# Performance work log

Hardware: AMD Instinct MI355X
Metric: run time of the kernel (lower is better)

Reference implementation:

```python
import jax, jax.numpy as jnp
import numpy as np

# LocalConv config (must match init_kwargs)
B, C, H, W = 64, 16, 64, 64
KH, KW = 3, 3
SH, SW = 1, 1
OUT_CH = 32
OH = (H - KH + SH) // SH  # 62
OW = (W - KW + SW) // SW  # 62
P = OH * OW               # 3844 positions
FEAT = C * KH * KW        # 144 (flatten order: C, kh, kw)


def setup_inputs() -> dict:
    key = jax.random.key(0)
    k1, k2 = jax.random.split(key)
    inputs = jax.random.normal(k1, (B, C, H, W), dtype=jnp.float32)
    kernel = jax.random.normal(k2, (P, FEAT, OUT_CH), dtype=jnp.float32)
    return {"inputs": inputs, "kernel": kernel}


def _extract_patches(x):
    # x: (B, C, H, W) -> (P, B, FEAT) with FEAT flattened as (C, kh, kw),
    # matching torch's reshape of inputs[:, :, i:i+kh, j:j+kw].
    i_idx = (jnp.arange(OH) * SH)[:, None] + jnp.arange(KH)[None, :]  # (OH, KH)
    j_idx = (jnp.arange(OW) * SW)[:, None] + jnp.arange(KW)[None, :]  # (OW, KW)
    # gather -> (B, C, OH, KH, OW, KW)
    p = x[:, :, i_idx[:, :, None, None], j_idx[None, None, :, :]]
    # -> (OH, OW, B, C, KH, KW)
    p = jnp.transpose(p, (2, 4, 0, 1, 3, 5))
    return p.reshape(P, B, FEAT)


def reference(inputs, kernel):
    patches = _extract_patches(inputs)                 # (P, B, FEAT)
    out = jnp.einsum('pbf,pfo->pbo', patches, kernel)  # per-position unshared matmul
    out = out.reshape(OH, OW, B, OUT_CH)
    return jnp.transpose(out, (2, 3, 0, 1))            # (B, OUT_CH, OH, OW)
```

## Files before the change

kernel.cpp:

```cpp
#include <hip/hip_runtime.h>

#define CIN    16
#define HH     64
#define WW     64
#define OHD    62
#define OWD    62
#define OUTC   32
#define FEATN  144
#define POUT   (OHD*OWD)
#define LSTRB  168
#define AR_W   18
#define AR_ELEMS   (3*AR_W*64*16)
#define BBUF_ELEMS (OUTC*LSTRB)
#define SMEM_BYTES ((AR_ELEMS + 2*BBUF_ELEMS)*2)

typedef __attribute__((ext_vector_type(8))) short  short8;
typedef __attribute__((ext_vector_type(4))) float  f32x4;
typedef __attribute__((ext_vector_type(2))) float  f32x2;

__device__ __forceinline__ unsigned short f2bf(float f) {
    unsigned int u = __float_as_uint(f);
    u += 0x7FFFu + ((u >> 16) & 1u);
    return (unsigned short)(u >> 16);
}

__device__ __forceinline__ void storeB4(unsigned short* Bb, int idx, f32x4 v) {
    int f   = idx >> 3;
    int o0  = (idx & 7) << 2;
    int c   = (f * 57) >> 9;
    int g   = f - 9 * c;
    int fpp = g * 16 + c;
    Bb[(o0 + 0) * LSTRB + fpp] = f2bf(v[0]);
    Bb[(o0 + 1) * LSTRB + fpp] = f2bf(v[1]);
    Bb[(o0 + 2) * LSTRB + fpp] = f2bf(v[2]);
    Bb[(o0 + 3) * LSTRB + fpp] = f2bf(v[3]);
}

template<int TW>
__device__ __forceinline__ void conv_body(
    const float* __restrict__ inp, const float* __restrict__ wgt,
    float* __restrict__ out, int oh, int ow0,
    unsigned short* __restrict__ Araw, unsigned short* __restrict__ B_lds)
{
    const int tid = threadIdx.x;
    constexpr int WTOT = TW + 2;

    for (int t = tid; t < 3 * 64 * WTOT; t += 512) {
        int w   = t % WTOT;
        int rem = t / WTOT;
        int b   = rem & 63;
        int kh  = rem >> 6;
        const float* src = inp + (size_t)b * (CIN * HH * WW)
                               + (size_t)(oh + kh) * WW + (ow0 + w);
        short8 h0, h1;
        #pragma unroll
        for (int c = 0; c < 8; ++c) h0[c] = (short)f2bf(src[(size_t)c * (HH * WW)]);
        #pragma unroll
        for (int c = 0; c < 8; ++c) h1[c] = (short)f2bf(src[(size_t)(c + 8) * (HH * WW)]);
        int s = (b >> 2) & 1;
        unsigned short* dst = Araw + ((kh * AR_W + w) * 64 + b) * 16;
        *(short8*)(dst + s * 8)       = h0;
        *(short8*)(dst + (1 - s) * 8) = h1;
    }

    for (int t = tid; t < 2 * OUTC * 16; t += 512) {
        int buf = t >> 9;
        int o   = (t >> 4) & 31;
        B_lds[buf * BBUF_ELEMS + o * LSTRB + 144 + (t & 15)] = 0;
    }

    const int p0 = oh * OWD + ow0;
    f32x4 wr0, wr1, wr2;
    auto issue = [&](int q) {
        const f32x4* src = (const f32x4*)(wgt + (size_t)(p0 + q) * (FEATN * OUTC));
        wr0 = src[tid];
        wr1 = src[512 + tid];
        if (tid < 128) wr2 = src[1024 + tid];
    };
    auto writeB = [&](unsigned short* Bb) {
        storeB4(Bb, tid, wr0);
        storeB4(Bb, 512 + tid, wr1);
        if (tid < 128) storeB4(Bb, 1024 + tid, wr2);
    };

    const int wid = tid >> 6, lane = tid & 63;
    const int fr  = lane & 15, fq = lane >> 4, fqh = fq >> 1;
    const int mt  = wid >> 1, nt = wid & 1;
    const int b   = mt * 16 + fr;
    const int c0e = (((fq & 1) ^ ((b >> 2) & 1)) << 3);
    int abase[5], boff[5];
    #pragma unroll
    for (int kc = 0; kc < 5; ++kc) {
        int g  = 2 * kc + fqh;
        int kh = (g * 11) >> 5;
        int kw = g - 3 * kh;
        abase[kc] = ((kh * AR_W + kw) * 64 + b) * 16 + c0e;
        boff[kc]  = (nt * 16 + fr) * LSTRB + kc * 32 + fq * 8;
    }

    issue(0);
    writeB(B_lds);
    issue(1);
    __syncthreads();

    f32x4 acc[TW];
    #pragma unroll
    for (int q = 0; q < TW; ++q) acc[q] = (f32x4){0.f, 0.f, 0.f, 0.f};

    #pragma unroll
    for (int q = 0; q < TW; ++q) {
        const unsigned short* Bc = B_lds + (q & 1) * BBUF_ELEMS;
        #pragma unroll
        for (int kc = 0; kc < 5; ++kc) {
            short8 a;
            if (kc == 4 && fqh == 1)
                a = (short8){0, 0, 0, 0, 0, 0, 0, 0};
            else
                a = *(const short8*)(Araw + abase[kc] + q * 1024);
            short8 bfr = *(const short8*)(Bc + boff[kc]);
            acc[q] = __builtin_amdgcn_mfma_f32_16x16x32_bf16(a, bfr, acc[q], 0, 0, 0);
        }
        if (q + 1 < TW) writeB(B_lds + ((q + 1) & 1) * BBUF_ELEMS);
        __syncthreads();
        if (q + 2 < TW) issue(q + 2);
    }

    const int o = nt * 16 + fr;
    #pragma unroll
    for (int r = 0; r < 4; ++r) {
        float* dst = out + ((size_t)((mt * 16 + fq * 4 + r) * OUTC + o)) * POUT
                         + (size_t)oh * OWD + ow0;
        #pragma unroll
        for (int j = 0; j < TW / 2; ++j) {
            f32x2 v = { acc[2 * j][r], acc[2 * j + 1][r] };
            *(f32x2*)(dst + 2 * j) = v;
        }
    }
}

__global__ __launch_bounds__(512) void localconv_kernel(
    const float* __restrict__ inp,
    const float* __restrict__ wgt,
    float* __restrict__ out)
{
    extern __shared__ unsigned short smem[];
    unsigned short* Araw  = smem;
    unsigned short* B_lds = smem + AR_ELEMS;

    const int l   = (blockIdx.x & 7) * 31 + (blockIdx.x >> 3);
    const int oh  = l >> 2;
    const int owt = l & 3;

    if (owt < 3) conv_body<16>(inp, wgt, out, oh, owt * 16, Araw, B_lds);
    else         conv_body<14>(inp, wgt, out, oh, 48, Araw, B_lds);
}

extern "C" void kernel_launch(void* const* d_in, const int* in_sizes, int n_in,
                              void* d_out, int out_size, void* d_ws, size_t ws_size,
                              hipStream_t stream) {
    const float* inp = (const float*)d_in[0];
    const float* wgt = (const float*)d_in[1];
    float* out = (float*)d_out;
    hipFuncSetAttribute((const void*)localconv_kernel,
                        hipFuncAttributeMaxDynamicSharedMemorySize, SMEM_BYTES);
    localconv_kernel<<<dim3(62 * 4), 512, SMEM_BYTES, stream>>>(inp, wgt, out);
}
```

Baseline: 39.44 us.

## Halve output-width tile, swizzle A in LDS, vectorize B staging, raise occupancy

Each block now covers 8 output columns instead of 16, so the grid doubles to 496 blocks and per-block LDS shrinks. The goal is better CU coverage and at least two resident blocks per CU, requested through launch_bounds(512,4). The A patch buffer gets an XOR swizzle on its 16-byte granules to reduce LDS bank conflicts. Weight staging is reorganized so each thread loads 8 scalars along the feature dimension and writes one 16-byte vector to LDS, replacing the scattered 2-byte stores. The costs are more halo rereads of the input per block and non-vectorized global weight loads, where each element is 288 floats apart per thread.

```diff
diff --git a/kernel.cpp b/kernel.cpp
--- a/kernel.cpp
+++ b/kernel.cpp
@@ -8,10 +8,10 @@
 #define OUTC   32
 #define FEATN  144
 #define POUT   (OHD*OWD)
-#define LSTRB  168
-#define AR_W   18
+#define LSTRB  152
+#define AR_W   10
 #define AR_ELEMS   (3*AR_W*64*16)
-#define BBUF_ELEMS (OUTC*LSTRB)
+#define BBUF_ELEMS (OUTC*LSTRB + 8)
 #define SMEM_BYTES ((AR_ELEMS + 2*BBUF_ELEMS)*2)
 
 typedef __attribute__((ext_vector_type(8))) short  short8;
@@ -24,18 +24,6 @@
     return (unsigned short)(u >> 16);
 }
 
-__device__ __forceinline__ void storeB4(unsigned short* Bb, int idx, f32x4 v) {
-    int f   = idx >> 3;
-    int o0  = (idx & 7) << 2;
-    int c   = (f * 57) >> 9;
-    int g   = f - 9 * c;
-    int fpp = g * 16 + c;
-    Bb[(o0 + 0) * LSTRB + fpp] = f2bf(v[0]);
-    Bb[(o0 + 1) * LSTRB + fpp] = f2bf(v[1]);
-    Bb[(o0 + 2) * LSTRB + fpp] = f2bf(v[2]);
-    Bb[(o0 + 3) * LSTRB + fpp] = f2bf(v[3]);
-}
-
 template<int TW>
 __device__ __forceinline__ void conv_body(
     const float* __restrict__ inp, const float* __restrict__ wgt,
@@ -45,7 +33,7 @@
     const int tid = threadIdx.x;
     constexpr int WTOT = TW + 2;
 
-    for (int t = tid; t < 3 * 64 * WTOT; t += 512) {
+    for (int t = tid; t < 3 * WTOT * 64; t += 512) {
         int w   = t % WTOT;
         int rem = t / WTOT;
         int b   = rem & 63;
@@ -54,48 +42,70 @@
                                + (size_t)(oh + kh) * WW + (ow0 + w);
         short8 h0, h1;
         #pragma unroll
-        for (int c = 0; c < 8; ++c) h0[c] = (short)f2bf(src[(size_t)c * (HH * WW)]);
+        for (int c = 0; c < 8; ++c) h0[c] = (short)f2bf(src[c * (HH * WW)]);
         #pragma unroll
-        for (int c = 0; c < 8; ++c) h1[c] = (short)f2bf(src[(size_t)(c + 8) * (HH * WW)]);
+        for (int c = 0; c < 8; ++c) h1[c] = (short)f2bf(src[(c + 8) * (HH * WW)]);
         int s = (b >> 2) & 1;
-        unsigned short* dst = Araw + ((kh * AR_W + w) * 64 + b) * 16;
-        *(short8*)(dst + s * 8)       = h0;
-        *(short8*)(dst + (1 - s) * 8) = h1;
+        unsigned Gb = (unsigned)(((kh * AR_W + w) * 64 + b) * 2);
+        unsigned wx = (unsigned)((w & 3) << 1);
+        *(short8*)(Araw + (((Gb + s) ^ wx) << 3))       = h0;
+        *(short8*)(Araw + (((Gb + (1 - s)) ^ wx) << 3)) = h1;
     }
 
-    for (int t = tid; t < 2 * OUTC * 16; t += 512) {
-        int buf = t >> 9;
-        int o   = (t >> 4) & 31;
-        B_lds[buf * BBUF_ELEMS + o * LSTRB + 144 + (t & 15)] = 0;
+    for (int t = tid; t < 2 * 264; t += 512) {
+        int buf = t / 264, r = t % 264;
+        int e = (r < 256) ? ((r >> 3) * LSTRB + 144 + (r & 7))
+                          : (OUTC * LSTRB + (r & 7));
+        B_lds[buf * BBUF_ELEMS + e] = 0;
     }
 
+    const int o_w   = tid & 31;
+    const int g_w   = (tid >> 6);
+    const int h_w   = (tid >> 5) & 1;
+    const int gbase  = (h_w * 72 + g_w) * 32 + o_w;
+    const int gbase2 = ((((tid >> 5) & 1) * 72 + 8) * 32) + o_w;
+    const int woff   = o_w * LSTRB + g_w * 16 + h_w * 8;
+    const int woff2  = o_w * LSTRB + 128 + ((tid >> 5) & 1) * 8;
     const int p0 = oh * OWD + ow0;
-    f32x4 wr0, wr1, wr2;
+
+    float wv[8], wv2[8];
     auto issue = [&](int q) {
-        const f32x4* src = (const f32x4*)(wgt + (size_t)(p0 + q) * (FEATN * OUTC));
-        wr0 = src[tid];
-        wr1 = src[512 + tid];
-        if (tid < 128) wr2 = src[1024 + tid];
+        const float* wp = wgt + (size_t)(p0 + q) * (FEATN * OUTC);
+        #pragma unroll
+        for (int j = 0; j < 8; ++j) wv[j] = wp[gbase + j * 288];
+        if (tid < 64) {
+            #pragma unroll
+            for (int j = 0; j < 8; ++j) wv2[j] = wp[gbase2 + j * 288];
+        }
     };
     auto writeB = [&](unsigned short* Bb) {
-        storeB4(Bb, tid, wr0);
-        storeB4(Bb, 512 + tid, wr1);
-        if (tid < 128) storeB4(Bb, 1024 + tid, wr2);
+        short8 sv;
+        #pragma unroll
+        for (int j = 0; j < 8; ++j) sv[j] = (short)f2bf(wv[j]);
+        *(short8*)(Bb + woff) = sv;
+        if (tid < 64) {
+            short8 sv2;
+            #pragma unroll
+            for (int j = 0; j < 8; ++j) sv2[j] = (short)f2bf(wv2[j]);
+            *(short8*)(Bb + woff2) = sv2;
+        }
     };
 
     const int wid = tid >> 6, lane = tid & 63;
-    const int fr  = lane & 15, fq = lane >> 4, fqh = fq >> 1;
-    const int mt  = wid >> 1, nt = wid & 1;
-    const int b   = mt * 16 + fr;
-    const int c0e = (((fq & 1) ^ ((b >> 2) & 1)) << 3);
-    int abase[5], boff[5];
+    const int fr = lane & 15, fq = lane >> 4, fqh = fq >> 1;
+    const int mt = wid >> 1, nt = wid & 1;
+    const int b  = mt * 16 + fr;
+    const int gr = (fq & 1) ^ ((b >> 2) & 1);
+    unsigned abase_g[5]; int kwv[5]; int boff[5];
     #pragma unroll
     for (int kc = 0; kc < 5; ++kc) {
         int g  = 2 * kc + fqh;
-        int kh = (g * 11) >> 5;
-        int kw = g - 3 * kh;
-        abase[kc] = ((kh * AR_W + kw) * 64 + b) * 16 + c0e;
-        boff[kc]  = (nt * 16 + fr) * LSTRB + kc * 32 + fq * 8;
+        int gc = (g > 8) ? 8 : g;
+        int kh = (gc * 11) >> 5;
+        int kw = gc - 3 * kh;
+        abase_g[kc] = (unsigned)(((kh * AR_W + kw) * 64 + b) * 2 + gr);
+        kwv[kc]     = kw;
+        boff[kc]    = (nt * 16 + fr) * LSTRB + kc * 32 + fq * 8;
     }
 
     issue(0);
@@ -113,12 +123,15 @@
         #pragma unroll
         for (int kc = 0; kc < 5; ++kc) {
             short8 a;
-            if (kc == 4 && fqh == 1)
+            if (kc == 4 && fqh == 1) {
                 a = (short8){0, 0, 0, 0, 0, 0, 0, 0};
-            else
-                a = *(const short8*)(Araw + abase[kc] + q * 1024);
-            short8 bfr = *(const short8*)(Bc + boff[kc]);
-            acc[q] = __builtin_amdgcn_mfma_f32_16x16x32_bf16(a, bfr, acc[q], 0, 0, 0);
+            } else {
+                unsigned gi = (abase_g[kc] + (unsigned)(q * 128))
+                              ^ (unsigned)(((q + kwv[kc]) & 3) << 1);
+                a = *(const short8*)(Araw + (gi << 3));
+            }
+            short8 bfv = *(const short8*)(Bc + boff[kc]);
+            acc[q] = __builtin_amdgcn_mfma_f32_16x16x32_bf16(a, bfv, acc[q], 0, 0, 0);
         }
         if (q + 1 < TW) writeB(B_lds + ((q + 1) & 1) * BBUF_ELEMS);
         __syncthreads();
@@ -138,7 +151,7 @@
     }
 }
 
-__global__ __launch_bounds__(512) void localconv_kernel(
+__global__ __launch_bounds__(512, 4) void localconv_kernel(
     const float* __restrict__ inp,
     const float* __restrict__ wgt,
     float* __restrict__ out)
@@ -147,12 +160,12 @@
     unsigned short* Araw  = smem;
     unsigned short* B_lds = smem + AR_ELEMS;
 
-    const int l   = (blockIdx.x & 7) * 31 + (blockIdx.x >> 3);
-    const int oh  = l >> 2;
-    const int owt = l & 3;
+    const int l   = (blockIdx.x & 7) * 62 + (blockIdx.x >> 3);
+    const int oh  = l >> 3;
+    const int owt = l & 7;
 
-    if (owt < 3) conv_body<16>(inp, wgt, out, oh, owt * 16, Araw, B_lds);
-    else         conv_body<14>(inp, wgt, out, oh, 48, Araw, B_lds);
+    if (owt < 7) conv_body<8>(inp, wgt, out, oh, owt * 8, Araw, B_lds);
+    else         conv_body<6>(inp, wgt, out, oh, 56, Araw, B_lds);
 }
 
 extern "C" void kernel_launch(void* const* d_in, const int* in_sizes, int n_in,
@@ -163,5 +176,5 @@
     float* out = (float*)d_out;
     hipFuncSetAttribute((const void*)localconv_kernel,
                         hipFuncAttributeMaxDynamicSharedMemorySize, SMEM_BYTES);
-    localconv_kernel<<<dim3(62 * 4), 512, SMEM_BYTES, stream>>>(inp, wgt, out);
+    localconv_kernel<<<dim3(62 * 8), 512, SMEM_BYTES, stream>>>(inp, wgt, out);
 }
```

New measurement: 37.57 us. 1.05x faster.
